# Kernel optimization log

Hardware: AMD Instinct MI355X
Metric: run time of the kernel (lower is better)

The kernel has to match this reference:

```python
import jax, jax.numpy as jnp
import numpy as np

# Module config (from init_kwargs)
KH, KW = 3, 3          # kernel_size
SH, SW = 2, 2          # stride
PH, PW = 1, 1          # padding
EPS = 1e-8             # temperature clamp eps
DEN_EPS = 1e-12        # denominator stabilizer (hardcoded in kornia)
DN = ('NCHW', 'OIHW', 'NCHW')


def _window_grid_kernel(kh, kw):
    # window coordinates residual to window center, normalized to [-1, 1]
    ys, xs = jnp.meshgrid(jnp.arange(kh, dtype=jnp.float32),
                          jnp.arange(kw, dtype=jnp.float32), indexing='ij')
    gx = xs * (2.0 / (kw - 1)) - 1.0
    gy = ys * (2.0 / (kh - 1)) - 1.0
    return jnp.stack([gx, gy], axis=0)[:, None]  # (2,1,kh,kw), ch0=x, ch1=y


def _center_kernel(kh, kw):
    k = jnp.zeros((2, 2, kh, kw), jnp.float32)
    k = k.at[0, 0, kh // 2, kw // 2].set(1.0)
    k = k.at[1, 1, kh // 2, kw // 2].set(1.0)
    return k  # (2,2,kh,kw)


def _sum_pool(x):
    # pool_coef * avg_pool2d(count_include_pad=True) == windowed sum with zero pad
    return jax.lax.reduce_window(x, 0.0, jax.lax.add,
                                 (1, 1, KH, KW), (1, 1, SH, SW),
                                 [(0, 0), (0, 0), (PH, PH), (PW, PW)])


def setup_inputs() -> dict:
    key = jax.random.key(0)
    x = jax.random.normal(key, (8, 16, 512, 512), dtype=jnp.float32)
    temperature = jnp.ones((), dtype=jnp.float32)
    return {"x": x, "temperature": temperature}


def reference(x, temperature):
    b, c, h, w = x.shape
    xf = x.reshape(b * c, 1, h, w)

    x_exp = jnp.exp(xf / jnp.maximum(temperature, EPS))

    den = _sum_pool(x_exp) + DEN_EPS                     # (BC,1,Ho,Wo)
    resp_maxima = _sum_pool(x_exp * xf) / den            # softmax-pooled values

    # weighted sum of window-relative coordinates
    coords_num = jax.lax.conv_general_dilated(
        x_exp, _window_grid_kernel(KH, KW), (SH, SW),
        [(PH, PH), (PW, PW)], dimension_numbers=DN)      # (BC,2,Ho,Wo)

    # global grid (x, y) pixel coordinates, center-picked per window
    ys, xs = jnp.meshgrid(jnp.arange(h, dtype=jnp.float32),
                          jnp.arange(w, dtype=jnp.float32), indexing='ij')
    grid_global = jnp.stack([xs, ys], axis=0)[None]      # (1,2,h,w)
    grid_pooled = jax.lax.conv_general_dilated(
        grid_global, _center_kernel(KH, KW), (SH, SW),
        [(PH, PH), (PW, PW)], dimension_numbers=DN)      # (1,2,Ho,Wo)

    coords_max = coords_num / den + grid_pooled          # broadcast over BC

    # normalized_coordinates=True: map pixel coords to [-1, 1]
    cx = coords_max[:, 0] * (2.0 / (w - 1)) - 1.0
    cy = coords_max[:, 1] * (2.0 / (h - 1)) - 1.0
    coords_max = jnp.stack([cx, cy], axis=1)             # (BC,2,Ho,Wo)

    return coords_max, resp_maxima
```

## Files before the change

kernel.cpp:

```cpp
#include <hip/hip_runtime.h>


#define H  512
#define W  512
#define HO 256
#define WO 256
#define BC 128

struct Acc { float den, numv, gx, gy; };

__device__ __forceinline__ void do_row(const float* __restrict__ row, int t,
                                       float mL, float k, float rs, Acc* a)
{
    float v[9];
    v[0] = row[t ? 8 * t - 1 : 0];
    float4 q1 = *(const float4*)(row + 8 * t);
    float4 q2 = *(const float4*)(row + 8 * t + 4);
    v[1] = q1.x; v[2] = q1.y; v[3] = q1.z; v[4] = q1.w;
    v[5] = q2.x; v[6] = q2.y; v[7] = q2.z; v[8] = q2.w;

    float e[9];
#pragma unroll
    for (int i = 0; i < 9; ++i) e[i] = __builtin_amdgcn_exp2f(k * v[i]);
    e[0] *= mL;

#pragma unroll
    for (int j = 0; j < 4; ++j) {
        float e0 = e[2 * j], e1 = e[2 * j + 1], e2 = e[2 * j + 2];
        float rsum = e0 + e1 + e2;
        a[j].den += rsum;
        a[j].gy   = fmaf(rs, rsum, a[j].gy);
        a[j].gx  += e2 - e0;
        a[j].numv = fmaf(e0, v[2 * j],
                    fmaf(e1, v[2 * j + 1],
                    fmaf(e2, v[2 * j + 2], a[j].numv)));
    }
}

__global__ __launch_bounds__(256) void casm_kernel(
    const float* __restrict__ x, const float* __restrict__ temp,
    float* __restrict__ out)
{
    int idx = blockIdx.x * 256 + threadIdx.x;
    int t  = idx & 63;
    int ho = (idx >> 6) & (HO - 1);
    int bc = idx >> 14;

    float k = 1.44269504088896340736f / fmaxf(temp[0], 1e-8f);
    float mL = t ? 1.0f : 0.0f;

    const float* __restrict__ xp = x + (size_t)bc * (H * W);
    int r0 = 2 * ho - 1;

    Acc a[4];
#pragma unroll
    for (int j = 0; j < 4; ++j) { a[j].den = 1e-12f; a[j].numv = 0.f; a[j].gx = 0.f; a[j].gy = 0.f; }

    if (r0 >= 0)
        do_row(xp + r0 * W,       t, mL, k, -1.0f, a);
    do_row(xp + (r0 + 1) * W,     t, mL, k,  0.0f, a);
    do_row(xp + (r0 + 2) * W,     t, mL, k,  1.0f, a);

    const float scale = 2.0f / 511.0f;
    float4 cx4, cy4, rp4;
    float* cxp = &cx4.x; float* cyp = &cy4.x; float* rpp = &rp4.x;
#pragma unroll
    for (int j = 0; j < 4; ++j) {
        float inv_den = __builtin_amdgcn_rcpf(a[j].den);
        int wo = 4 * t + j;
        cxp[j] = (a[j].gx * inv_den + (float)(2 * wo)) * scale - 1.0f;
        cyp[j] = (a[j].gy * inv_den + (float)(2 * ho)) * scale - 1.0f;
        rpp[j] = a[j].numv * inv_den;
    }

    size_t pix   = (size_t)ho * WO + 4 * t;
    size_t cbase = (size_t)bc * (2 * HO * WO) + pix;
    *(float4*)(out + cbase)            = cx4;
    *(float4*)(out + cbase + HO * WO)  = cy4;
    *(float4*)(out + (size_t)BC * 2 * HO * WO + (size_t)bc * HO * WO + pix) = rp4;
}

extern "C" void kernel_launch(void* const* d_in, const int* in_sizes, int n_in,
                              void* d_out, int out_size, void* d_ws, size_t ws_size,
                              hipStream_t stream) {
    const float* x    = (const float*)d_in[0];
    const float* temp = (const float*)d_in[1];
    float* out        = (float*)d_out;

    int total  = BC * HO * (WO / 4);
    int blocks = total / 256;
    casm_kernel<<<blocks, 256, 0, stream>>>(x, temp, out);
}
```

Measured before the change: 219.8 us.

## Compute two output rows per thread, sharing the overlapping input row, with nontemporal stores

Each thread now produces two vertically adjacent output rows from five input rows instead of one output row from three. The shared middle row is loaded and exponentiated once and reused by both outputs. This cuts redundant global loads and exp work by roughly a sixth. Outputs are written with nontemporal stores to avoid polluting cache, at the cost of half as many threads and more registers per thread.

New measurement: 223.4 us. Within noise of the previous version (+1.6%).

```diff
diff --git a/kernel.cpp b/kernel.cpp
--- a/kernel.cpp
+++ b/kernel.cpp
@@ -7,23 +7,14 @@
 #define WO 256
 #define BC 128
 
+typedef float f32x4 __attribute__((ext_vector_type(4)));
+
 struct Acc { float den, numv, gx, gy; };
 
-__device__ __forceinline__ void do_row(const float* __restrict__ row, int t,
-                                       float mL, float k, float rs, Acc* a)
+__device__ __forceinline__ void accum_row(const float* __restrict__ v,
+                                          const float* __restrict__ e,
+                                          float rs, Acc* __restrict__ a)
 {
-    float v[9];
-    v[0] = row[t ? 8 * t - 1 : 0];
-    float4 q1 = *(const float4*)(row + 8 * t);
-    float4 q2 = *(const float4*)(row + 8 * t + 4);
-    v[1] = q1.x; v[2] = q1.y; v[3] = q1.z; v[4] = q1.w;
-    v[5] = q2.x; v[6] = q2.y; v[7] = q2.z; v[8] = q2.w;
-
-    float e[9];
-#pragma unroll
-    for (int i = 0; i < 9; ++i) e[i] = __builtin_amdgcn_exp2f(k * v[i]);
-    e[0] *= mL;
-
 #pragma unroll
     for (int j = 0; j < 4; ++j) {
         float e0 = e[2 * j], e1 = e[2 * j + 1], e2 = e[2 * j + 2];
@@ -43,41 +34,81 @@
 {
     int idx = blockIdx.x * 256 + threadIdx.x;
     int t  = idx & 63;
-    int ho = (idx >> 6) & (HO - 1);
-    int bc = idx >> 14;
+    int hp = (idx >> 6) & 127;
+    int bc = idx >> 13;
 
-    float k = 1.44269504088896340736f / fmaxf(temp[0], 1e-8f);
+    float k  = 1.44269504088896340736f / fmaxf(temp[0], 1e-8f);
     float mL = t ? 1.0f : 0.0f;
 
     const float* __restrict__ xp = x + (size_t)bc * (H * W);
-    int r0 = 2 * ho - 1;
+    int r0 = 4 * hp - 1;
+    float m0 = (r0 >= 0) ? 1.0f : 0.0f;
 
-    Acc a[4];
+    float v[5][9];
 #pragma unroll
-    for (int j = 0; j < 4; ++j) { a[j].den = 1e-12f; a[j].numv = 0.f; a[j].gx = 0.f; a[j].gy = 0.f; }
+    for (int rr = 0; rr < 5; ++rr) {
+        int r = r0 + rr;
+        const float* __restrict__ row = xp + (r < 0 ? 0 : r) * W;
+        v[rr][0] = row[t ? 8 * t - 1 : 0];
+        f32x4 q1 = *(const f32x4*)(row + 8 * t);
+        f32x4 q2 = *(const f32x4*)(row + 8 * t + 4);
+        v[rr][1] = q1.x; v[rr][2] = q1.y; v[rr][3] = q1.z; v[rr][4] = q1.w;
+        v[rr][5] = q2.x; v[rr][6] = q2.y; v[rr][7] = q2.z; v[rr][8] = q2.w;
+    }
 
-    if (r0 >= 0)
-        do_row(xp + r0 * W,       t, mL, k, -1.0f, a);
-    do_row(xp + (r0 + 1) * W,     t, mL, k,  0.0f, a);
-    do_row(xp + (r0 + 2) * W,     t, mL, k,  1.0f, a);
+    Acc A[4], B[4];
+#pragma unroll
+    for (int j = 0; j < 4; ++j) {
+        A[j].den = 1e-12f; A[j].numv = 0.f; A[j].gx = 0.f; A[j].gy = 0.f;
+        B[j].den = 1e-12f; B[j].numv = 0.f; B[j].gx = 0.f; B[j].gy = 0.f;
+    }
+
+    float e[9];
+#pragma unroll
+    for (int i = 0; i < 9; ++i) e[i] = m0 * __builtin_amdgcn_exp2f(k * v[0][i]);
+    e[0] *= mL;
+    accum_row(v[0], e, -1.0f, A);
+#pragma unroll
+    for (int i = 0; i < 9; ++i) e[i] = __builtin_amdgcn_exp2f(k * v[1][i]);
+    e[0] *= mL;
+    accum_row(v[1], e, 0.0f, A);
+#pragma unroll
+    for (int i = 0; i < 9; ++i) e[i] = __builtin_amdgcn_exp2f(k * v[2][i]);
+    e[0] *= mL;
+    accum_row(v[2], e,  1.0f, A);
+    accum_row(v[2], e, -1.0f, B);
+#pragma unroll
+    for (int i = 0; i < 9; ++i) e[i] = __builtin_amdgcn_exp2f(k * v[3][i]);
+    e[0] *= mL;
+    accum_row(v[3], e, 0.0f, B);
+#pragma unroll
+    for (int i = 0; i < 9; ++i) e[i] = __builtin_amdgcn_exp2f(k * v[4][i]);
+    e[0] *= mL;
+    accum_row(v[4], e, 1.0f, B);
 
     const float scale = 2.0f / 511.0f;
-    float4 cx4, cy4, rp4;
-    float* cxp = &cx4.x; float* cyp = &cy4.x; float* rpp = &rp4.x;
+    size_t cstride = (size_t)HO * WO;
+    size_t obase   = (size_t)bc * (2 * cstride);
+    size_t rbase   = (size_t)BC * 2 * cstride + (size_t)bc * cstride;
+
 #pragma unroll
-    for (int j = 0; j < 4; ++j) {
-        float inv_den = __builtin_amdgcn_rcpf(a[j].den);
-        int wo = 4 * t + j;
-        cxp[j] = (a[j].gx * inv_den + (float)(2 * wo)) * scale - 1.0f;
-        cyp[j] = (a[j].gy * inv_den + (float)(2 * ho)) * scale - 1.0f;
-        rpp[j] = a[j].numv * inv_den;
+    for (int rr = 0; rr < 2; ++rr) {
+        Acc* a = rr ? B : A;
+        int ho = 2 * hp + rr;
+        f32x4 cx4, cy4, rp4;
+#pragma unroll
+        for (int j = 0; j < 4; ++j) {
+            float inv_den = __builtin_amdgcn_rcpf(a[j].den);
+            int wo = 4 * t + j;
+            cx4[j] = (a[j].gx * inv_den + (float)(2 * wo)) * scale - 1.0f;
+            cy4[j] = (a[j].gy * inv_den + (float)(2 * ho)) * scale - 1.0f;
+            rp4[j] = a[j].numv * inv_den;
+        }
+        size_t pix = (size_t)ho * WO + 4 * t;
+        __builtin_nontemporal_store(cx4, (f32x4*)(out + obase + pix));
+        __builtin_nontemporal_store(cy4, (f32x4*)(out + obase + cstride + pix));
+        __builtin_nontemporal_store(rp4, (f32x4*)(out + rbase + pix));
     }
-
-    size_t pix   = (size_t)ho * WO + 4 * t;
-    size_t cbase = (size_t)bc * (2 * HO * WO) + pix;
-    *(float4*)(out + cbase)            = cx4;
-    *(float4*)(out + cbase + HO * WO)  = cy4;
-    *(float4*)(out + (size_t)BC * 2 * HO * WO + (size_t)bc * HO * WO + pix) = rp4;
 }
 
 extern "C" void kernel_launch(void* const* d_in, const int* in_sizes, int n_in,
@@ -87,7 +118,7 @@
     const float* temp = (const float*)d_in[1];
     float* out        = (float*)d_out;
 
-    int total  = BC * HO * (WO / 4);
+    int total  = BC * (HO / 2) * (WO / 4);
     int blocks = total / 256;
     casm_kernel<<<blocks, 256, 0, stream>>>(x, temp, out);
 }
```
